# Kernel optimization log

Hardware: AMD Instinct MI355X
Metric: run time of the kernel (lower is better)

## Reference

```python
import jax, jax.numpy as jnp
import numpy as np

IM_SIZE = (32, 32)
SCALE = float(IM_SIZE[0] * IM_SIZE[1])  # sqrt((x*y)^2) = x*y


def setup_inputs() -> dict:
    key = jax.random.key(0)
    k1, k2, k3 = jax.random.split(key, 3)
    b, n, p, x, y, d = 8, 8, 64, IM_SIZE[0], IM_SIZE[1], 8
    shape = (b, n, p, x, y, d)
    return {
        "query": jax.random.normal(k1, shape, dtype=jnp.float32),
        "key": jax.random.normal(k2, shape, dtype=jnp.float32),
        "value": jax.random.normal(k3, shape, dtype=jnp.float32),
        "key_padding_mask": jnp.zeros((b, p), dtype=bool),
    }


def reference(query, key, value, key_padding_mask):
    # scores: contract over spatial (x,y) and channel (d) dims -> [b,n,p,q]
    scores = jnp.einsum('bnpxyd,bnqxyd->bnpq', query, key) / SCALE
    if key_padding_mask is not None:
        mask = key_padding_mask[:, None, None, :]  # [b,1,1,q]
        scores = jnp.where(mask, -jnp.inf, scores)
    attn = jax.nn.softmax(scores, axis=-1)  # [b,n,p,q]
    out = jnp.einsum('bnpq,bnqxyd->bnpxyd', attn, value)
    # permute(0,2,3,4,5,1) -> [b,p,x,y,d,n]
    return jnp.transpose(out, (0, 2, 3, 4, 5, 1))
```

## Files before the change

### kernel.cpp

```cpp
#include <hip/hip_runtime.h>
#include <hip/hip_bf16.h>
#include <cstdint>
#include <cstddef>


typedef __attribute__((ext_vector_type(4))) float f32x4;
typedef __attribute__((ext_vector_type(8))) short bf16x8;
typedef __attribute__((ext_vector_type(4))) short shortx4;

__device__ __forceinline__ unsigned short f2bf(float x) {
    unsigned int u = __builtin_bit_cast(unsigned int, x);
    u += 0x7FFFu + ((u >> 16) & 1u);
    return (unsigned short)(u >> 16);
}

__device__ __forceinline__ bf16x8 pack8(float4 lo, float4 hi) {
    bf16x8 f;
    f[0] = (short)f2bf(lo.x); f[1] = (short)f2bf(lo.y);
    f[2] = (short)f2bf(lo.z); f[3] = (short)f2bf(lo.w);
    f[4] = (short)f2bf(hi.x); f[5] = (short)f2bf(hi.y);
    f[6] = (short)f2bf(hi.z); f[7] = (short)f2bf(hi.w);
    return f;
}

__global__ __launch_bounds__(1024) void qk_mfma_kernel(
    const float* __restrict__ Q, const float* __restrict__ K,
    float* __restrict__ partial, int clen)
{
    __shared__ unsigned short Qs[64 * 256];
    __shared__ unsigned short Ks[64 * 256];

    const int bn   = blockIdx.x;
    const int ch   = blockIdx.y;
    const int tid  = threadIdx.x;
    const int w    = tid >> 6;
    const int lane = tid & 63;
    const int wr   = w >> 2;
    const int wc   = w & 3;
    const int frow = lane & 15;
    const int kg   = lane >> 4;

    const float* Qb = Q + (size_t)bn * 64 * 8192 + (size_t)ch * clen;
    const float* Kb = K + (size_t)bn * 64 * 8192 + (size_t)ch * clen;

    const int srow = tid >> 4;
    const int sc   = (tid & 15) * 16;
    const int nph  = clen >> 8;

    f32x4 acc = (f32x4)(0.f);
    const int arow = wr * 16 + frow;
    const int brow = wc * 16 + frow;

    #pragma unroll 1
    for (int ph = 0; ph < nph; ++ph) {
        const float4* qp = (const float4*)(Qb + (size_t)srow * 8192 + ph * 256 + sc);
        const float4* kp = (const float4*)(Kb + (size_t)srow * 8192 + ph * 256 + sc);
        const float4 q0 = qp[0], q1 = qp[1], q2 = qp[2], q3 = qp[3];
        const float4 k0 = kp[0], k1 = kp[1], k2 = kp[2], k3 = kp[3];
        if (ph) __syncthreads();
        const int sl0 = ((tid & 15) * 2    ) ^ (srow & 7);
        const int sl1 = ((tid & 15) * 2 + 1) ^ (srow & 7);
        *(bf16x8*)(Qs + srow * 256 + sl0 * 8) = pack8(q0, q1);
        *(bf16x8*)(Qs + srow * 256 + sl1 * 8) = pack8(q2, q3);
        *(bf16x8*)(Ks + srow * 256 + sl0 * 8) = pack8(k0, k1);
        *(bf16x8*)(Ks + srow * 256 + sl1 * 8) = pack8(k2, k3);
        __syncthreads();
        #pragma unroll
        for (int ks = 0; ks < 8; ++ks) {
            const bf16x8 a = *(const bf16x8*)(Qs + arow * 256 +
                                (((ks * 4 + kg) ^ (arow & 7)) * 8));
            const bf16x8 b = *(const bf16x8*)(Ks + brow * 256 +
                                (((ks * 4 + kg) ^ (brow & 7)) * 8));
            acc = __builtin_amdgcn_mfma_f32_16x16x32_bf16(a, b, acc, 0, 0, 0);
        }
    }

    float* pb = partial + ((size_t)ch * 64 + bn) * 4096;
    const int p0 = wr * 16 + kg * 4;
    const int q0 = wc * 16 + frow;
    #pragma unroll
    for (int r = 0; r < 4; ++r)
        pb[(size_t)(p0 + r) * 64 + q0] = acc[r];
}

__global__ __launch_bounds__(256) void softmax_kernel(
    float* __restrict__ ws, const unsigned char* __restrict__ mask, int kchunks)
{
    const int row  = blockIdx.x * 4 + (threadIdx.x >> 6);
    const int q    = threadIdx.x & 63;
    float s = 0.f;
    for (int c = 0; c < kchunks; ++c)
        s += ws[((size_t)c * 4096 + row) * 64 + q];
    s *= (1.0f / 1024.0f);
    const int b = row >> 9;
    if (mask[b * 64 + q]) s = -__builtin_inff();
    float m = s;
    #pragma unroll
    for (int off = 32; off; off >>= 1) m = fmaxf(m, __shfl_xor(m, off));
    const float e = __expf(s - m);
    float sum = e;
    #pragma unroll
    for (int off = 32; off; off >>= 1) sum += __shfl_xor(sum, off);
    ws[(size_t)row * 64 + q] = e / sum;
}

__global__ __launch_bounds__(512, 2) void pv_mfma_kernel(
    const float* __restrict__ V, const float* __restrict__ attn,
    float* __restrict__ out)
{
    __shared__ unsigned char smem[65536];

    const int b     = blockIdx.y;
    const int chunk = blockIdx.x;
    const int tid   = threadIdx.x;
    const int w     = tid >> 6;
    const int lane  = tid & 63;

    const float* Vb = V    + (size_t)(b * 8 + w) * 64 * 8192 + (size_t)chunk * 64;
    const float* Ab = attn + (size_t)(b * 8 + w) * 4096;

    unsigned short* vtn = (unsigned short*)smem + w * 4096;

    const int c  = lane >> 2;
    const int qg = lane & 3;
    #pragma unroll
    for (int s = 0; s < 4; ++s) {
        const int q0 = s * 16 + qg * 4;
        const float4 r0 = *(const float4*)&Vb[(size_t)(q0 + 0) * 8192 + c * 4];
        const float4 r1 = *(const float4*)&Vb[(size_t)(q0 + 1) * 8192 + c * 4];
        const float4 r2 = *(const float4*)&Vb[(size_t)(q0 + 2) * 8192 + c * 4];
        const float4 r3 = *(const float4*)&Vb[(size_t)(q0 + 3) * 8192 + c * 4];
        const float v0[4] = {r0.x, r0.y, r0.z, r0.w};
        const float v1[4] = {r1.x, r1.y, r1.z, r1.w};
        const float v2[4] = {r2.x, r2.y, r2.z, r2.w};
        const float v3[4] = {r3.x, r3.y, r3.z, r3.w};
        #pragma unroll
        for (int cc = 0; cc < 4; ++cc) {
            const int row = c * 4 + cc;
            shortx4 pk;
            pk.x = (short)f2bf(v0[cc]);
            pk.y = (short)f2bf(v1[cc]);
            pk.z = (short)f2bf(v2[cc]);
            pk.w = (short)f2bf(v3[cc]);
            const int soff = row * 64 + (q0 ^ ((row & 7) << 3) ^ (((row >> 3) & 3) << 4));
            *(shortx4*)(vtn + soff) = pk;
        }
    }

    const int arow = lane & 15;
    const int q0a  = (lane >> 4) * 8;
    bf16x8 afrag[4][2];
    #pragma unroll
    for (int mt = 0; mt < 4; ++mt) {
        #pragma unroll
        for (int ks = 0; ks < 2; ++ks) {
            const float* ap = Ab + (mt * 16 + arow) * 64 + ks * 32 + q0a;
            const float4 lo = *(const float4*)ap;
            const float4 hi = *(const float4*)(ap + 4);
            afrag[mt][ks] = pack8(lo, hi);
        }
    }

    f32x4 acc[4][4];
    #pragma unroll
    for (int mt = 0; mt < 4; ++mt)
        #pragma unroll
        for (int nt = 0; nt < 4; ++nt)
            acc[mt][nt] = (f32x4)(0.f);

    const int bcol = lane & 15;
    const int q0b  = (lane >> 4) * 8;
    #pragma unroll
    for (int nt = 0; nt < 4; ++nt) {
        bf16x8 bfr[2];
        #pragma unroll
        for (int ks = 0; ks < 2; ++ks) {
            const int row  = nt * 16 + bcol;
            const int q0   = ks * 32 + q0b;
            const int soff = row * 64 + (q0 ^ ((row & 7) << 3) ^ (((row >> 3) & 3) << 4));
            bfr[ks] = *(const bf16x8*)(vtn + soff);
        }
        #pragma unroll
        for (int ks = 0; ks < 2; ++ks)
            #pragma unroll
            for (int mt = 0; mt < 4; ++mt)
                acc[mt][nt] = __builtin_amdgcn_mfma_f32_16x16x32_bf16(
                    afrag[mt][ks], bfr[ks], acc[mt][nt], 0, 0, 0);
    }

    float* ob = (float*)smem;
    const int pq = lane >> 4;
    const int pl = tid >> 5;
    const int g  = tid & 31;
    #pragma unroll
    for (int mt = 0; mt < 4; ++mt) {
        __syncthreads();
        #pragma unroll
        for (int nt = 0; nt < 4; ++nt)
            #pragma unroll
            for (int r = 0; r < 4; ++r) {
                const int prow = pq * 4 + r;
                const int xc   = nt * 16 + (lane & 15);
                ob[prow * 576 + xc * 9 + w] = acc[mt][nt][r];
            }
        __syncthreads();
        float* orow = out + (size_t)b * 4194304 + (size_t)(mt * 16 + pl) * 65536
                          + (size_t)chunk * 512;
        #pragma unroll
        for (int u = 0; u < 4; ++u) {
            const int f0 = g * 4 + u * 128;
            float4 vv;
            vv.x = ob[pl * 576 + ((f0 + 0) >> 3) * 9 + ((f0 + 0) & 7)];
            vv.y = ob[pl * 576 + ((f0 + 1) >> 3) * 9 + ((f0 + 1) & 7)];
            vv.z = ob[pl * 576 + ((f0 + 2) >> 3) * 9 + ((f0 + 2) & 7)];
            vv.w = ob[pl * 576 + ((f0 + 3) >> 3) * 9 + ((f0 + 3) & 7)];
            *(float4*)&orow[f0] = vv;
        }
    }
}

extern "C" void kernel_launch(void* const* d_in, const int* in_sizes, int n_in,
                              void* d_out, int out_size, void* d_ws, size_t ws_size,
                              hipStream_t stream)
{
    const float* Q = (const float*)d_in[0];
    const float* K = (const float*)d_in[1];
    const float* V = (const float*)d_in[2];
    const unsigned char* mask = (const unsigned char*)d_in[3];
    float* out = (float*)d_out;
    float* ws  = (float*)d_ws;

    int kchunks = 32;
    while (kchunks > 1 &&
           (size_t)kchunks * 4096 * 64 * sizeof(float) > ws_size)
        kchunks >>= 1;
    const int clen = 8192 / kchunks;

    qk_mfma_kernel<<<dim3(64, kchunks), 1024, 0, stream>>>(Q, K, ws, clen);
    softmax_kernel<<<1024, 256, 0, stream>>>(ws, mask, kchunks);
    pv_mfma_kernel<<<dim3(128, 8), 512, 0, stream>>>(V, ws, out);
}
```

Before: 141.7 us.

## Pre-pack Q/K to swizzled bf16 tiles and stream them into LDS

Adds a repack kernel that converts Q and K to bf16 once and stores them in the output buffer as pre-swizzled per-chunk tiles. The QK kernel then fills LDS straight from global memory with global_load_lds, with no in-kernel conversion or loop. The aim is to take the fp32-to-bf16 packing and register staging out of the QK kernel. In exchange it adds a full extra pass over Q and K (fp32 read plus bf16 write and re-read) and an extra launch. It also hardcodes 32 K-chunks, dropping the check against workspace size.

```diff
diff --git a/kernel.cpp b/kernel.cpp
--- a/kernel.cpp
+++ b/kernel.cpp
@@ -23,61 +23,84 @@
     return f;
 }
 
+__device__ __forceinline__ void gload16(const float* g,
+    __attribute__((address_space(3))) float* l)
+{
+    __builtin_amdgcn_global_load_lds(
+        (const __attribute__((address_space(1))) unsigned int*)(uintptr_t)g,
+        (__attribute__((address_space(3))) unsigned int*)l, 16, 0, 0);
+}
+
+__global__ __launch_bounds__(256) void repack_kernel(
+    const float* __restrict__ Q, const float* __restrict__ K,
+    unsigned short* __restrict__ t)
+{
+    const int bn  = blockIdx.x;
+    const int rg  = blockIdx.y;
+    const int qk  = blockIdx.z;
+    const int tid = threadIdx.x;
+    const float* src = (qk ? K : Q) + (size_t)bn * 64 * 8192;
+    unsigned short* dstb = t + ((size_t)bn * 64 + qk) * 16384;
+
+    const int ch = tid >> 3;
+    const int s0 = (tid & 7) * 4;
+
+    #pragma unroll 1
+    for (int r = 0; r < 8; ++r) {
+        const int row = rg * 8 + r;
+        const float4* p = (const float4*)(src + (size_t)row * 8192 + tid * 32);
+        float4 v[8];
+        #pragma unroll
+        for (int j = 0; j < 8; ++j) v[j] = p[j];
+        unsigned short* trow = dstb + (size_t)ch * 2 * 16384 + row * 256;
+        #pragma unroll
+        for (int j2 = 0; j2 < 4; ++j2) {
+            const int s = (s0 + j2) ^ (row & 7);
+            *(bf16x8*)(trow + s * 8) = pack8(v[2 * j2], v[2 * j2 + 1]);
+        }
+    }
+}
+
 __global__ __launch_bounds__(1024) void qk_mfma_kernel(
-    const float* __restrict__ Q, const float* __restrict__ K,
-    float* __restrict__ partial, int clen)
-{
-    __shared__ unsigned short Qs[64 * 256];
-    __shared__ unsigned short Ks[64 * 256];
+    const unsigned short* __restrict__ t, float* __restrict__ partial)
+{
+    __shared__ unsigned short tile[2][16384];
 
     const int bn   = blockIdx.x;
     const int ch   = blockIdx.y;
     const int tid  = threadIdx.x;
     const int w    = tid >> 6;
     const int lane = tid & 63;
-    const int wr   = w >> 2;
-    const int wc   = w & 3;
     const int frow = lane & 15;
     const int kg   = lane >> 4;
 
-    const float* Qb = Q + (size_t)bn * 64 * 8192 + (size_t)ch * clen;
-    const float* Kb = K + (size_t)bn * 64 * 8192 + (size_t)ch * clen;
-
-    const int srow = tid >> 4;
-    const int sc   = (tid & 15) * 16;
-    const int nph  = clen >> 8;
+    const float* src = (const float*)(t + ((size_t)bn * 32 + ch) * 2 * 16384);
+    auto l3 = (__attribute__((address_space(3))) float*)(uintptr_t)&tile[0][0];
+
+    #pragma unroll
+    for (int i = 0; i < 4; ++i) {
+        const int c = w * 4 + i;
+        gload16(src + c * 256 + lane * 4, l3 + c * 256 + lane * 4);
+    }
+    __syncthreads();
 
     f32x4 acc = (f32x4)(0.f);
-    const int arow = wr * 16 + frow;
-    const int brow = wc * 16 + frow;
-
-    #pragma unroll 1
-    for (int ph = 0; ph < nph; ++ph) {
-        const float4* qp = (const float4*)(Qb + (size_t)srow * 8192 + ph * 256 + sc);
-        const float4* kp = (const float4*)(Kb + (size_t)srow * 8192 + ph * 256 + sc);
-        const float4 q0 = qp[0], q1 = qp[1], q2 = qp[2], q3 = qp[3];
-        const float4 k0 = kp[0], k1 = kp[1], k2 = kp[2], k3 = kp[3];
-        if (ph) __syncthreads();
-        const int sl0 = ((tid & 15) * 2    ) ^ (srow & 7);
-        const int sl1 = ((tid & 15) * 2 + 1) ^ (srow & 7);
-        *(bf16x8*)(Qs + srow * 256 + sl0 * 8) = pack8(q0, q1);
-        *(bf16x8*)(Qs + srow * 256 + sl1 * 8) = pack8(q2, q3);
-        *(bf16x8*)(Ks + srow * 256 + sl0 * 8) = pack8(k0, k1);
-        *(bf16x8*)(Ks + srow * 256 + sl1 * 8) = pack8(k2, k3);
-        __syncthreads();
-        #pragma unroll
-        for (int ks = 0; ks < 8; ++ks) {
-            const bf16x8 a = *(const bf16x8*)(Qs + arow * 256 +
-                                (((ks * 4 + kg) ^ (arow & 7)) * 8));
-            const bf16x8 b = *(const bf16x8*)(Ks + brow * 256 +
-                                (((ks * 4 + kg) ^ (brow & 7)) * 8));
-            acc = __builtin_amdgcn_mfma_f32_16x16x32_bf16(a, b, acc, 0, 0, 0);
-        }
+    const int arow = (w >> 2) * 16 + frow;
+    const int brow = (w & 3) * 16 + frow;
+    const unsigned short* Qs = tile[0];
+    const unsigned short* Ks = tile[1];
+    #pragma unroll
+    for (int ks = 0; ks < 8; ++ks) {
+        const bf16x8 a = *(const bf16x8*)(Qs + arow * 256 +
+                            (((ks * 4 + kg) ^ (arow & 7)) * 8));
+        const bf16x8 b = *(const bf16x8*)(Ks + brow * 256 +
+                            (((ks * 4 + kg) ^ (brow & 7)) * 8));
+        acc = __builtin_amdgcn_mfma_f32_16x16x32_bf16(a, b, acc, 0, 0, 0);
     }
 
     float* pb = partial + ((size_t)ch * 64 + bn) * 4096;
-    const int p0 = wr * 16 + kg * 4;
-    const int q0 = wc * 16 + frow;
+    const int p0 = (w >> 2) * 16 + kg * 4;
+    const int q0 = (w & 3) * 16 + frow;
     #pragma unroll
     for (int r = 0; r < 4; ++r)
         pb[(size_t)(p0 + r) * 64 + q0] = acc[r];
@@ -230,13 +253,12 @@
     float* out = (float*)d_out;
     float* ws  = (float*)d_ws;
 
-    int kchunks = 32;
-    while (kchunks > 1 &&
-           (size_t)kchunks * 4096 * 64 * sizeof(float) > ws_size)
-        kchunks >>= 1;
-    const int clen = 8192 / kchunks;
-
-    qk_mfma_kernel<<<dim3(64, kchunks), 1024, 0, stream>>>(Q, K, ws, clen);
+    unsigned short* tiles = (unsigned short*)d_out;
+
+    const int kchunks = 32;
+
+    repack_kernel<<<dim3(64, 8, 2), 256, 0, stream>>>(Q, K, tiles);
+    qk_mfma_kernel<<<dim3(64, 32), 1024, 0, stream>>>(tiles, ws);
     softmax_kernel<<<1024, 256, 0, stream>>>(ws, mask, kchunks);
     pv_mfma_kernel<<<dim3(128, 8), 512, 0, stream>>>(V, ws, out);
 }
```

Result: slower. 197.8 us (+39.6%).
